# Kernel tuning notes

Measured on AMD Instinct MI355X. Metric: run time of the kernel, lower is better.

The kernel has to match this reference:

```python
import jax, jax.numpy as jnp
import numpy as np

N_NEIGHBORS = 30
TEMPERATURE = 0.07


def _weight_matrix(n, n_neigh):
    # Analytic form of the O(N) python-loop banded weight matrix:
    # for d = j - i:
    #   d == 0            -> 0
    #   0 < d < n_neigh   -> d / n_neigh
    #   d >= n_neigh      -> 1
    #   -n_neigh <= d < 0 -> (-d - 1) / n_neigh
    #   d < -n_neigh      -> 1
    idx = jnp.arange(n)
    d = idx[None, :] - idx[:, None]
    slope = jnp.float32(1.0 / n_neigh)
    right = jnp.minimum(d.astype(jnp.float32) * slope, 1.0)
    left = jnp.where(d >= -n_neigh, (-d - 1).astype(jnp.float32) * slope, 1.0)
    return jnp.where(d >= 0, right, left)


def _l2_normalize(x, eps=1e-12):
    # matches torch.nn.functional.normalize (norm clamped to eps)
    n = jnp.linalg.norm(x, axis=-1, keepdims=True)
    return x / jnp.maximum(n, eps)


def setup_inputs() -> dict:
    key = jax.random.key(0)
    k1, k2 = jax.random.split(key)
    B2, D, L = 16, 256, 256  # 2*batch, embed dim, seq len -> N = 2*8*256 = 4096
    embeddings = jax.random.normal(k1, (B2, D, L), dtype=jnp.float32)
    masks = jnp.zeros((B2, L), dtype=bool)
    labelvecs = jax.random.randint(k2, (B2, L), 0, 20)
    return {"embeddings": embeddings, "masks": masks, "labelvecs": labelvecs}


def reference(embeddings, masks, labelvecs):
    B2, D, L = embeddings.shape
    b = B2 // 2
    f1 = embeddings[:b].transpose(0, 2, 1).reshape(b * L, D)  # cat(unbind(transpose))
    f2 = embeddings[b:].transpose(0, 2, 1).reshape(b * L, D)
    f1 = _l2_normalize(f1)
    f2 = _l2_normalize(f2)
    all_pairs = jnp.concatenate([f1, f2], axis=0)  # [N, D], N = 2*b*L
    N = all_pairs.shape[0]
    M = b * L

    sims = jnp.matmul(all_pairs, all_pairs.T)  # [N, N]
    w = _weight_matrix(N, N_NEIGHBORS)
    e = jnp.exp(sims / TEMPERATURE) * w
    probs = e / jnp.sum(e, axis=1, keepdims=True)

    # pair_labels = eye(M).repeat(2,2) with zeroed diagonal -> [[0, I], [I, 0]],
    # exactly one positive per row at column (i + M) % N; row sums are 1.
    rows = jnp.arange(N)
    partner = (rows + M) % N
    mean_pos = jnp.take_along_axis(probs, partner[:, None], axis=1)[:, 0]
    return jnp.mean(mean_pos)
```

## Files before the change

### kernel.cpp

```cpp
#include <hip/hip_runtime.h>
#include <stdint.h>

#define N_TOTAL 4096
#define DIMS 256
#define M_HALF 2048
#define NNEIGH 30

typedef __bf16 bf16_t;
typedef bf16_t bf16x8 __attribute__((ext_vector_type(8)));
typedef float f32x4 __attribute__((ext_vector_type(4)));

typedef __attribute__((address_space(3))) uint32_t lds_u32;
typedef const __attribute__((address_space(1))) uint32_t glb_u32;

__device__ inline uint16_t f2bf(float f) {
    union { float f; uint32_t u; } v; v.f = f;
    uint32_t u = v.u;
    uint32_t r = (u + 0x7fffu + ((u >> 16) & 1u)) >> 16;
    return (uint16_t)r;
}

__global__ __launch_bounds__(256) void nt_kernel(const float* __restrict__ emb,
                                                 uint16_t* __restrict__ F,
                                                 float* __restrict__ den) {
    __shared__ float tile[16][257];
    __shared__ float invn[16];
    const int bi = blockIdx.x >> 4;
    const int lc = blockIdx.x & 15;
    const int l0 = lc * 16;
    const int tid = threadIdx.x;
    if (tid < 16) den[blockIdx.x * 16 + tid] = 0.f;
    const float* src = emb + (size_t)bi * DIMS * 256 + l0;
    #pragma unroll
    for (int p = 0; p < 16; ++p) {
        int idx = p * 256 + tid;
        int l = idx & 15;
        int d = idx >> 4;
        tile[l][d] = src[(size_t)d * 256 + l];
    }
    __syncthreads();
    {
        int l = tid >> 4;
        int c = tid & 15;
        float ss = 0.f;
        #pragma unroll
        for (int d = 0; d < 256; d += 16) {
            float v = tile[l][d + c];
            ss += v * v;
        }
        ss += __shfl_xor(ss, 1, 64);
        ss += __shfl_xor(ss, 2, 64);
        ss += __shfl_xor(ss, 4, 64);
        ss += __shfl_xor(ss, 8, 64);
        if (c == 0) invn[l] = 1.0f / fmaxf(sqrtf(ss), 1e-12f);
    }
    __syncthreads();
    #pragma unroll
    for (int p = 0; p < 16; ++p) {
        int r = bi * 256 + l0 + p;
        F[(size_t)r * DIMS + tid] = f2bf(tile[p][tid] * invn[p]);
    }
}

__device__ inline void stage_tile(const uint16_t* __restrict__ F, char* smem,
                                  int buf, int k0, int rowA0, int rowB0, int tid) {
    const int wid = tid >> 6;
    #pragma unroll
    for (int i = 0; i < 4; ++i) {
        int p = i * 256 + tid;
        int row = p >> 3;
        int pc = p & 7;
        int c = pc ^ (row & 7);
        const uint16_t* ga = F + (size_t)(rowA0 + row) * DIMS + k0 + c * 8;
        char* la = smem + buf * 32768 + i * 4096 + wid * 1024;
        __builtin_amdgcn_global_load_lds((glb_u32*)ga, (lds_u32*)la, 16, 0, 0);
    }
    #pragma unroll
    for (int i = 0; i < 4; ++i) {
        int p = i * 256 + tid;
        int row = p >> 3;
        int pc = p & 7;
        int c = pc ^ (row & 7);
        const uint16_t* gb = F + (size_t)(rowB0 + row) * DIMS + k0 + c * 8;
        char* lb = smem + buf * 32768 + 16384 + i * 4096 + wid * 1024;
        __builtin_amdgcn_global_load_lds((glb_u32*)gb, (lds_u32*)lb, 16, 0, 0);
    }
}

__global__ __launch_bounds__(256) void sim_kernel(const uint16_t* __restrict__ F,
                                                  float* __restrict__ den,
                                                  float* __restrict__ num) {
    __shared__ char smem[65536];
    const int tid = threadIdx.x;
    const int wid = tid >> 6;
    const int lane = tid & 63;
    const int lr = lane & 15;
    const int kg = lane >> 4;
    const int wr = wid >> 1, wc = wid & 1;

    const int bid = blockIdx.x;
    const int swz = (bid & 7) * 128 + (bid >> 3);
    const int bm = swz >> 5, bn = swz & 31;
    const int rowA0 = bm * 128, rowB0 = bn * 128;

    f32x4 acc[4][4];
    #pragma unroll
    for (int a = 0; a < 4; ++a)
        #pragma unroll
        for (int b = 0; b < 4; ++b) acc[a][b] = (f32x4){0.f, 0.f, 0.f, 0.f};

    stage_tile(F, smem, 0, 0, rowA0, rowB0, tid);
    __syncthreads();

    for (int t = 0; t < 4; ++t) {
        const int cur = t & 1;
        if (t < 3) stage_tile(F, smem, cur ^ 1, (t + 1) * 64, rowA0, rowB0, tid);
        const char* Ab = smem + cur * 32768;
        const char* Bb = Ab + 16384;
        #pragma unroll
        for (int kk = 0; kk < 2; ++kk) {
            bf16x8 af[4], bfr[4];
            #pragma unroll
            for (int a = 0; a < 4; ++a) {
                int r = wr * 64 + a * 16 + lr;
                int pc = (kk * 4 + kg) ^ (r & 7);
                af[a] = *(const bf16x8*)(Ab + r * 128 + pc * 16);
            }
            #pragma unroll
            for (int b = 0; b < 4; ++b) {
                int r = wc * 64 + b * 16 + lr;
                int pc = (kk * 4 + kg) ^ (r & 7);
                bfr[b] = *(const bf16x8*)(Bb + r * 128 + pc * 16);
            }
            #pragma unroll
            for (int a = 0; a < 4; ++a)
                #pragma unroll
                for (int b = 0; b < 4; ++b)
                    acc[a][b] = __builtin_amdgcn_mfma_f32_16x16x32_bf16(af[a], bfr[b], acc[a][b], 0, 0, 0);
        }
        __syncthreads();
    }

    const int i0 = rowA0 + wr * 64;
    const int j0 = rowB0 + wc * 64;
    const float invT = 1.0f / 0.07f;
    const float slope = 1.0f / (float)NNEIGH;
    float rs[4][4];
    #pragma unroll
    for (int a = 0; a < 4; ++a)
        #pragma unroll
        for (int e = 0; e < 4; ++e) rs[a][e] = 0.f;

    #pragma unroll
    for (int a = 0; a < 4; ++a) {
        #pragma unroll
        for (int b = 0; b < 4; ++b) {
            const int col = j0 + b * 16 + lr;
            #pragma unroll
            for (int e = 0; e < 4; ++e) {
                const int row = i0 + a * 16 + kg * 4 + e;
                const int d = col - row;
                float wv = (d >= 0) ? fminf((float)d * slope, 1.0f)
                                    : ((d >= -NNEIGH) ? (float)(-d - 1) * slope : 1.0f);
                float v = __expf(acc[a][b][e] * invT) * wv;
                rs[a][e] += v;
                int pc = row + M_HALF;
                if (pc >= N_TOTAL) pc -= N_TOTAL;
                if (col == pc) num[row] = v;
            }
        }
    }
    #pragma unroll
    for (int a = 0; a < 4; ++a)
        #pragma unroll
        for (int e = 0; e < 4; ++e) {
            float s = rs[a][e];
            s += __shfl_xor(s, 1, 64);
            s += __shfl_xor(s, 2, 64);
            s += __shfl_xor(s, 4, 64);
            s += __shfl_xor(s, 8, 64);
            if (lr == 0) atomicAdd(&den[i0 + a * 16 + kg * 4 + e], s);
        }
}

__global__ __launch_bounds__(256) void fin_kernel(const float* __restrict__ num,
                                                  const float* __restrict__ den,
                                                  float* __restrict__ out) {
    __shared__ float sbuf[4];
    const int tid = threadIdx.x;
    float s = 0.f;
    for (int i = tid; i < N_TOTAL; i += 256) s += num[i] / den[i];
    s += __shfl_xor(s, 1, 64);
    s += __shfl_xor(s, 2, 64);
    s += __shfl_xor(s, 4, 64);
    s += __shfl_xor(s, 8, 64);
    s += __shfl_xor(s, 16, 64);
    s += __shfl_xor(s, 32, 64);
    if ((tid & 63) == 0) sbuf[tid >> 6] = s;
    __syncthreads();
    if (tid == 0) out[0] = (sbuf[0] + sbuf[1] + sbuf[2] + sbuf[3]) * (1.0f / (float)N_TOTAL);
}

extern "C" void kernel_launch(void* const* d_in, const int* in_sizes, int n_in,
                              void* d_out, int out_size, void* d_ws, size_t ws_size,
                              hipStream_t stream) {
    const float* emb = (const float*)d_in[0];
    uint16_t* F = (uint16_t*)d_ws;
    float* den = (float*)((char*)d_ws + (size_t)N_TOTAL * DIMS * sizeof(uint16_t));
    float* num = den + N_TOTAL;

    nt_kernel<<<dim3(256), dim3(256), 0, stream>>>(emb, F, den);
    sim_kernel<<<dim3(1024), dim3(256), 0, stream>>>(F, den, num);
    fin_kernel<<<dim3(1), dim3(256), 0, stream>>>(num, den, (float*)d_out);
}
```

Before: 44.01 us.

## Exploit symmetry of similarity matrix to compute only upper-triangle tiles

The similarity matrix is symmetric, so the kernel now launches only the upper-triangular 128x128 tile pairs (528 instead of 1024). Off-diagonal tiles add the row-sum contribution and a transposed column-sum contribution with the mirrored weight to the denominator. They also write the partner numerator for both the row and the column. Diagonal tiles stage only one operand. This roughly halves MFMA and load work, at the cost of extra exp-weighted accumulation, more atomics per tile, and a serial loop to decode the triangle index.

```diff
diff --git a/kernel.cpp b/kernel.cpp
--- a/kernel.cpp
+++ b/kernel.cpp
@@ -5,6 +5,8 @@
 #define DIMS 256
 #define M_HALF 2048
 #define NNEIGH 30
+#define NBLK 32
+#define NTRI 528
 
 typedef __bf16 bf16_t;
 typedef bf16_t bf16x8 __attribute__((ext_vector_type(8)));
@@ -63,7 +65,8 @@
 }
 
 __device__ inline void stage_tile(const uint16_t* __restrict__ F, char* smem,
-                                  int buf, int k0, int rowA0, int rowB0, int tid) {
+                                  int buf, int k0, int rowA0, int rowB0, int tid,
+                                  bool stageB) {
     const int wid = tid >> 6;
     #pragma unroll
     for (int i = 0; i < 4; ++i) {
@@ -75,15 +78,17 @@
         char* la = smem + buf * 32768 + i * 4096 + wid * 1024;
         __builtin_amdgcn_global_load_lds((glb_u32*)ga, (lds_u32*)la, 16, 0, 0);
     }
-    #pragma unroll
-    for (int i = 0; i < 4; ++i) {
-        int p = i * 256 + tid;
-        int row = p >> 3;
-        int pc = p & 7;
-        int c = pc ^ (row & 7);
-        const uint16_t* gb = F + (size_t)(rowB0 + row) * DIMS + k0 + c * 8;
-        char* lb = smem + buf * 32768 + 16384 + i * 4096 + wid * 1024;
-        __builtin_amdgcn_global_load_lds((glb_u32*)gb, (lds_u32*)lb, 16, 0, 0);
+    if (stageB) {
+        #pragma unroll
+        for (int i = 0; i < 4; ++i) {
+            int p = i * 256 + tid;
+            int row = p >> 3;
+            int pc = p & 7;
+            int c = pc ^ (row & 7);
+            const uint16_t* gb = F + (size_t)(rowB0 + row) * DIMS + k0 + c * 8;
+            char* lb = smem + buf * 32768 + 16384 + i * 4096 + wid * 1024;
+            __builtin_amdgcn_global_load_lds((glb_u32*)gb, (lds_u32*)lb, 16, 0, 0);
+        }
     }
 }
 
@@ -99,8 +104,11 @@
     const int wr = wid >> 1, wc = wid & 1;
 
     const int bid = blockIdx.x;
-    const int swz = (bid & 7) * 128 + (bid >> 3);
-    const int bm = swz >> 5, bn = swz & 31;
+    int t = (bid & 7) * 66 + (bid >> 3);
+    int bm = 0, rem = NBLK;
+    while (t >= rem) { t -= rem; ++bm; --rem; }
+    const int bn = bm + t;
+    const bool diag = (bm == bn);
     const int rowA0 = bm * 128, rowB0 = bn * 128;
 
     f32x4 acc[4][4];
@@ -109,14 +117,15 @@
         #pragma unroll
         for (int b = 0; b < 4; ++b) acc[a][b] = (f32x4){0.f, 0.f, 0.f, 0.f};
 
-    stage_tile(F, smem, 0, 0, rowA0, rowB0, tid);
-    __syncthreads();
-
-    for (int t = 0; t < 4; ++t) {
-        const int cur = t & 1;
-        if (t < 3) stage_tile(F, smem, cur ^ 1, (t + 1) * 64, rowA0, rowB0, tid);
+    stage_tile(F, smem, 0, 0, rowA0, rowB0, tid, !diag);
+    __syncthreads();
+
+    const int bOff = diag ? 0 : 16384;
+    for (int tt = 0; tt < 4; ++tt) {
+        const int cur = tt & 1;
+        if (tt < 3) stage_tile(F, smem, cur ^ 1, (tt + 1) * 64, rowA0, rowB0, tid, !diag);
         const char* Ab = smem + cur * 32768;
-        const char* Bb = Ab + 16384;
+        const char* Bb = Ab + bOff;
         #pragma unroll
         for (int kk = 0; kk < 2; ++kk) {
             bf16x8 af[4], bfr[4];
@@ -151,23 +160,50 @@
         #pragma unroll
         for (int e = 0; e < 4; ++e) rs[a][e] = 0.f;
 
-    #pragma unroll
-    for (int a = 0; a < 4; ++a) {
+    if (diag) {
+        #pragma unroll
+        for (int a = 0; a < 4; ++a) {
+            #pragma unroll
+            for (int b = 0; b < 4; ++b) {
+                const int col = j0 + b * 16 + lr;
+                #pragma unroll
+                for (int e = 0; e < 4; ++e) {
+                    const int row = i0 + a * 16 + kg * 4 + e;
+                    const int d = col - row;
+                    float wv = (d >= 0) ? fminf((float)d * slope, 1.0f)
+                                        : ((d >= -NNEIGH) ? (float)(-d - 1) * slope : 1.0f);
+                    rs[a][e] += __expf(acc[a][b][e] * invT) * wv;
+                }
+            }
+        }
+    } else {
+        float cs[4];
+        #pragma unroll
+        for (int b = 0; b < 4; ++b) cs[b] = 0.f;
+        #pragma unroll
+        for (int a = 0; a < 4; ++a) {
+            #pragma unroll
+            for (int b = 0; b < 4; ++b) {
+                const int col = j0 + b * 16 + lr;
+                #pragma unroll
+                for (int e = 0; e < 4; ++e) {
+                    const int row = i0 + a * 16 + kg * 4 + e;
+                    const int d = col - row;
+                    float ex = __expf(acc[a][b][e] * invT);
+                    float wrow = fminf((float)d * slope, 1.0f);
+                    float wcol = (d <= NNEIGH) ? (float)(d - 1) * slope : 1.0f;
+                    rs[a][e] += ex * wrow;
+                    cs[b] += ex * wcol;
+                    if (d == M_HALF) { num[row] = ex; num[col] = ex; }
+                }
+            }
+        }
         #pragma unroll
         for (int b = 0; b < 4; ++b) {
-            const int col = j0 + b * 16 + lr;
-            #pragma unroll
-            for (int e = 0; e < 4; ++e) {
-                const int row = i0 + a * 16 + kg * 4 + e;
-                const int d = col - row;
-                float wv = (d >= 0) ? fminf((float)d * slope, 1.0f)
-                                    : ((d >= -NNEIGH) ? (float)(-d - 1) * slope : 1.0f);
-                float v = __expf(acc[a][b][e] * invT) * wv;
-                rs[a][e] += v;
-                int pc = row + M_HALF;
-                if (pc >= N_TOTAL) pc -= N_TOTAL;
-                if (col == pc) num[row] = v;
-            }
+            float s = cs[b];
+            s += __shfl_xor(s, 16, 64);
+            s += __shfl_xor(s, 32, 64);
+            if (kg == 0) atomicAdd(&den[j0 + b * 16 + lr], s);
         }
     }
     #pragma unroll
@@ -210,6 +246,6 @@
     float* num = den + N_TOTAL;
 
     nt_kernel<<<dim3(256), dim3(256), 0, stream>>>(emb, F, den);
-    sim_kernel<<<dim3(1024), dim3(256), 0, stream>>>(F, den, num);
+    sim_kernel<<<dim3(NTRI), dim3(256), 0, stream>>>(F, den, num);
     fin_kernel<<<dim3(1), dim3(256), 0, stream>>>(num, den, (float*)d_out);
 }
```

Measured after the change: 46.81 us. +6.4%, slower.

## Use 8 waves per sim block and simplify the epilogue weight and exp math

Applied to the files above, without the earlier changes.

Doubles the sim kernel's block to 512 threads. Each of the 8 waves now computes a 64x32 sub-tile, so per-wave accumulators fall from 16 to 8 MFMA fragments and tile staging is split across more threads. The epilogue computes the banded weight branch-free through an absolute-value trick and uses exp2f with a prescaled constant. The partner check is also gated by a per-block flag, so most blocks skip it. The aim is more waves for latency hiding and cheaper epilogue ALU work, at the cost of re-reading each A fragment from LDS in more waves.

```diff
diff --git a/kernel.cpp b/kernel.cpp
--- a/kernel.cpp
+++ b/kernel.cpp
@@ -5,6 +5,7 @@
 #define DIMS 256
 #define M_HALF 2048
 #define NNEIGH 30
+#define NTILES 1024
 
 typedef __bf16 bf16_t;
 typedef bf16_t bf16x8 __attribute__((ext_vector_type(8)));
@@ -62,64 +63,64 @@
     }
 }
 
-__device__ inline void stage_tile(const uint16_t* __restrict__ F, char* smem,
-                                  int buf, int k0, int rowA0, int rowB0, int tid) {
+__device__ inline void stage512(const uint16_t* __restrict__ F, char* smem,
+                                int buf, int k0, int rowA0, int rowB0, int tid) {
     const int wid = tid >> 6;
     #pragma unroll
-    for (int i = 0; i < 4; ++i) {
-        int p = i * 256 + tid;
+    for (int i = 0; i < 2; ++i) {
+        int p = i * 512 + tid;
         int row = p >> 3;
         int pc = p & 7;
         int c = pc ^ (row & 7);
         const uint16_t* ga = F + (size_t)(rowA0 + row) * DIMS + k0 + c * 8;
-        char* la = smem + buf * 32768 + i * 4096 + wid * 1024;
+        char* la = smem + buf * 32768 + i * 8192 + wid * 1024;
         __builtin_amdgcn_global_load_lds((glb_u32*)ga, (lds_u32*)la, 16, 0, 0);
     }
     #pragma unroll
-    for (int i = 0; i < 4; ++i) {
-        int p = i * 256 + tid;
+    for (int i = 0; i < 2; ++i) {
+        int p = i * 512 + tid;
         int row = p >> 3;
         int pc = p & 7;
         int c = pc ^ (row & 7);
         const uint16_t* gb = F + (size_t)(rowB0 + row) * DIMS + k0 + c * 8;
-        char* lb = smem + buf * 32768 + 16384 + i * 4096 + wid * 1024;
+        char* lb = smem + buf * 32768 + 16384 + i * 8192 + wid * 1024;
         __builtin_amdgcn_global_load_lds((glb_u32*)gb, (lds_u32*)lb, 16, 0, 0);
     }
 }
 
-__global__ __launch_bounds__(256) void sim_kernel(const uint16_t* __restrict__ F,
-                                                  float* __restrict__ den,
-                                                  float* __restrict__ num) {
+__global__ __launch_bounds__(512, 2) void sim_kernel(const uint16_t* __restrict__ F,
+                                                     float* __restrict__ den,
+                                                     float* __restrict__ num) {
     __shared__ char smem[65536];
     const int tid = threadIdx.x;
     const int wid = tid >> 6;
     const int lane = tid & 63;
     const int lr = lane & 15;
     const int kg = lane >> 4;
-    const int wr = wid >> 1, wc = wid & 1;
+    const int wr = wid >> 2, wc = wid & 3;
 
     const int bid = blockIdx.x;
     const int swz = (bid & 7) * 128 + (bid >> 3);
     const int bm = swz >> 5, bn = swz & 31;
     const int rowA0 = bm * 128, rowB0 = bn * 128;
 
-    f32x4 acc[4][4];
+    f32x4 acc[4][2];
     #pragma unroll
     for (int a = 0; a < 4; ++a)
         #pragma unroll
-        for (int b = 0; b < 4; ++b) acc[a][b] = (f32x4){0.f, 0.f, 0.f, 0.f};
-
-    stage_tile(F, smem, 0, 0, rowA0, rowB0, tid);
+        for (int bb = 0; bb < 2; ++bb) acc[a][bb] = (f32x4){0.f, 0.f, 0.f, 0.f};
+
+    stage512(F, smem, 0, 0, rowA0, rowB0, tid);
     __syncthreads();
 
     for (int t = 0; t < 4; ++t) {
         const int cur = t & 1;
-        if (t < 3) stage_tile(F, smem, cur ^ 1, (t + 1) * 64, rowA0, rowB0, tid);
+        if (t < 3) stage512(F, smem, cur ^ 1, (t + 1) * 64, rowA0, rowB0, tid);
         const char* Ab = smem + cur * 32768;
         const char* Bb = Ab + 16384;
         #pragma unroll
         for (int kk = 0; kk < 2; ++kk) {
-            bf16x8 af[4], bfr[4];
+            bf16x8 af[4], bfr[2];
             #pragma unroll
             for (int a = 0; a < 4; ++a) {
                 int r = wr * 64 + a * 16 + lr;
@@ -127,24 +128,25 @@
                 af[a] = *(const bf16x8*)(Ab + r * 128 + pc * 16);
             }
             #pragma unroll
-            for (int b = 0; b < 4; ++b) {
-                int r = wc * 64 + b * 16 + lr;
+            for (int bb = 0; bb < 2; ++bb) {
+                int r = wc * 32 + bb * 16 + lr;
                 int pc = (kk * 4 + kg) ^ (r & 7);
-                bfr[b] = *(const bf16x8*)(Bb + r * 128 + pc * 16);
+                bfr[bb] = *(const bf16x8*)(Bb + r * 128 + pc * 16);
             }
             #pragma unroll
             for (int a = 0; a < 4; ++a)
                 #pragma unroll
-                for (int b = 0; b < 4; ++b)
-                    acc[a][b] = __builtin_amdgcn_mfma_f32_16x16x32_bf16(af[a], bfr[b], acc[a][b], 0, 0, 0);
+                for (int bb = 0; bb < 2; ++bb)
+                    acc[a][bb] = __builtin_amdgcn_mfma_f32_16x16x32_bf16(af[a], bfr[bb], acc[a][bb], 0, 0, 0);
         }
         __syncthreads();
     }
 
     const int i0 = rowA0 + wr * 64;
-    const int j0 = rowB0 + wc * 64;
-    const float invT = 1.0f / 0.07f;
+    const int j0 = rowB0 + wc * 32;
+    const float K2 = 1.442695041f / 0.07f;
     const float slope = 1.0f / (float)NNEIGH;
+    const bool hasPartner = (((bn - bm) & 31) == 16);
     float rs[4][4];
     #pragma unroll
     for (int a = 0; a < 4; ++a)
@@ -154,19 +156,17 @@
     #pragma unroll
     for (int a = 0; a < 4; ++a) {
         #pragma unroll
-        for (int b = 0; b < 4; ++b) {
-            const int col = j0 + b * 16 + lr;
+        for (int bb = 0; bb < 2; ++bb) {
+            const int col = j0 + bb * 16 + lr;
             #pragma unroll
             for (int e = 0; e < 4; ++e) {
                 const int row = i0 + a * 16 + kg * 4 + e;
                 const int d = col - row;
-                float wv = (d >= 0) ? fminf((float)d * slope, 1.0f)
-                                    : ((d >= -NNEIGH) ? (float)(-d - 1) * slope : 1.0f);
-                float v = __expf(acc[a][b][e] * invT) * wv;
+                const int dm = d ^ (d >> 31);
+                float wv = fminf((float)dm * slope, 1.0f);
+                float v = exp2f(acc[a][bb][e] * K2) * wv;
                 rs[a][e] += v;
-                int pc = row + M_HALF;
-                if (pc >= N_TOTAL) pc -= N_TOTAL;
-                if (col == pc) num[row] = v;
+                if (hasPartner && ((d & (N_TOTAL - 1)) == M_HALF)) num[row] = v;
             }
         }
     }
@@ -208,8 +208,9 @@
     uint16_t* F = (uint16_t*)d_ws;
     float* den = (float*)((char*)d_ws + (size_t)N_TOTAL * DIMS * sizeof(uint16_t));
     float* num = den + N_TOTAL;
+    float* out = (float*)d_out;
 
     nt_kernel<<<dim3(256), dim3(256), 0, stream>>>(emb, F, den);
-    sim_kernel<<<dim3(1024), dim3(256), 0, stream>>>(F, den, num);
-    fin_kernel<<<dim3(1), dim3(256), 0, stream>>>(num, den, (float*)d_out);
-}
+    sim_kernel<<<dim3(NTILES), dim3(512), 0, stream>>>(F, den, num);
+    fin_kernel<<<dim3(1), dim3(256), 0, stream>>>(num, den, out);
+}
```

After: 65.56 us. 1.49x slower.
